# Kernel optimization log

Measured on AMD Instinct MI355X. Metric: run time of the kernel, lower is better.

## Reference

```python
import jax, jax.numpy as jnp
import numpy as np
from jax import lax

SUR_BETA = 4.0
THRESH = 1.0
ALPHA = float(np.exp(-1.0 / 20.0))  # membrane decay, tau_mem=20
BETA = float(np.exp(-1.0 / 5.0))    # synaptic decay, tau_syn=5

@jax.custom_vjp
def spike(x):
    return (x >= 0).astype(jnp.float32)

def _spike_fwd(x):
    return spike(x), x

def _spike_bwd(x, g):
    e = jnp.exp(-SUR_BETA * jnp.abs(x))
    sg = SUR_BETA * e / (2.0 * (1.0 + e) ** 2)
    return (g * sg,)

spike.defvjp(_spike_fwd, _spike_bwd)

def lif_layer(x, W, b):
    # x: [B, T, Din] -> spikes [B, T, H]
    xt = jnp.einsum('bti,ih->bth', x, W) + b
    B, T, H = xt.shape
    z = jnp.zeros((B, H), xt.dtype)
    def step(carry, x_t):
        v, i = carry
        i = BETA * i + x_t
        v = ALPHA * v + i
        s = spike(v - THRESH)
        v = v * (1.0 - s)  # multiplicative reset
        return (v, i), s
    _, sp = lax.scan(step, (z, z), xt.transpose(1, 0, 2))
    return sp.transpose(1, 0, 2)

def layer_norm(x, scale, bias, eps=1e-6):
    m = jnp.mean(x, axis=-1, keepdims=True)
    v = jnp.mean((x - m) ** 2, axis=-1, keepdims=True)
    return (x - m) / jnp.sqrt(v + eps) * scale + bias

def setup_inputs() -> dict:
    key = jax.random.key(0)
    ks = jax.random.split(key, 6)
    B, T, S, F = 64, 512, 64, 16
    D = S * F  # 1024
    def w(k, shape, fan):
        return (jax.random.normal(k, shape, jnp.float32) / np.sqrt(fan)).astype(jnp.float32)
    return dict(
        spike_trains=(jax.random.uniform(ks[0], (B, T, S, F)) < 0.2).astype(jnp.float32),
        W0=w(ks[1], (D, 256), D), b0=jnp.zeros((256,), jnp.float32),
        W1=w(ks[2], (256, 128), 256), b1=jnp.zeros((128,), jnp.float32),
        W2=w(ks[3], (128, 64), 128), b2=jnp.zeros((64,), jnp.float32),
        ln1_scale=jnp.ones((256,), jnp.float32), ln1_bias=jnp.zeros((256,), jnp.float32),
        ln2_scale=jnp.ones((128,), jnp.float32), ln2_bias=jnp.zeros((128,), jnp.float32),
        Wc=w(ks[4], (B, 2), B), bc=jnp.zeros((2,), jnp.float32),
    )

def reference(spike_trains, W0, b0, W1, b1, W2, b2,
              ln1_scale, ln1_bias, ln2_scale, ln2_bias, Wc, bc):
    B, T, S, F = spike_trains.shape
    x = spike_trains.reshape(B, T, S * F)
    x = lif_layer(x, W0, b0)                                   # [B,T,256]
    x = lif_layer(layer_norm(x, ln1_scale, ln1_bias), W1, b1)  # [B,T,128]
    x = lif_layer(layer_norm(x, ln2_scale, ln2_bias), W2, b2)  # [B,T,64]
    pooled = jnp.mean(x, axis=(1, 2))  # [B]  (faithful to source: mean over time AND hidden)
    logits = pooled @ Wc + bc          # [num_classes] -- classifier sees batch as feature dim
    return (logits, pooled, jnp.mean(x))
```

## Files before the change

### kernel.cpp

```cpp
#include <hip/hip_runtime.h>

#define T_STEPS 512
#define BATCH 64

__device__ constexpr float ALPHA_ = 0.95122942450071400910f;
__device__ constexpr float BETA_  = 0.81873075307798185867f;

typedef __attribute__((ext_vector_type(8))) short bf16x8;
typedef __attribute__((ext_vector_type(4))) float f32x4;

__device__ inline unsigned short f2bf_rne(float f) {
  union { float f; unsigned int u; } v{f};
  const unsigned int u = v.u;
  return (unsigned short)((u + 0x7FFFu + ((u >> 16) & 1u)) >> 16);
}
__device__ inline float bf2f(unsigned short h) {
  union { unsigned int u; float f; } v{(unsigned int)h << 16};
  return v.f;
}

__device__ inline void gload16(const void* g, void* l) {
  __builtin_amdgcn_global_load_lds(
      (const __attribute__((address_space(1))) unsigned int*)g,
      (__attribute__((address_space(3))) unsigned int*)l, 16, 0, 0);
}

__device__ inline bf16x8 cvt8_trunc(f32x4 a, f32x4 b) {
  bf16x8 r;
  const unsigned int* ua = (const unsigned int*)&a;
  const unsigned int* ub = (const unsigned int*)&b;
  r[0] = (short)(ua[0] >> 16); r[1] = (short)(ua[1] >> 16);
  r[2] = (short)(ua[2] >> 16); r[3] = (short)(ua[3] >> 16);
  r[4] = (short)(ub[0] >> 16); r[5] = (short)(ub[1] >> 16);
  r[6] = (short)(ub[2] >> 16); r[7] = (short)(ub[3] >> 16);
  return r;
}

template <int BN, bool A_F32, bool LNFOLD>
__global__ __launch_bounds__(256) void gemm_mfma(
    const void* __restrict__ Av, const char* __restrict__ Bhi,
    const char* __restrict__ Blo, const float* __restrict__ uvec,
    const float* __restrict__ cvec, const float* __restrict__ invv,
    const float* __restrict__ miv, float* __restrict__ C,
    int M, int N, int K) {
  constexpr int NFPW = BN / 32;
  constexpr int UB = BN * 4;
  __shared__ char As[8192];
  __shared__ char Bh[UB * 16];
  __shared__ char Bl[UB * 16];

  const int tid = threadIdx.x;
  const int lane = tid & 63;
  const int wave = tid >> 6;
  const int wr = wave >> 1, wc = wave & 1;
  const int l15 = lane & 15, l4 = lane >> 4;
  const int row0 = blockIdx.y * 128;
  const int col0 = blockIdx.x * BN;
  const int KB = K / 32;
  const int cbKB = blockIdx.x * KB;

  f32x4 acc[4][NFPW] = {};

  for (int kb = 0; kb < KB; ++kb) {
    const int k0 = kb * 32;
    f32x4 a0lo, a0hi, a1lo, a1hi;
    if constexpr (A_F32) {
      const float* A = (const float*)Av;
      const int r0 = tid >> 2, j0 = tid & 3;
      const float* p0 = A + (size_t)(row0 + r0) * K + k0 + j0 * 8;
      const float* p1 = A + (size_t)(row0 + 64 + r0) * K + k0 + j0 * 8;
      a0lo = *(const f32x4*)p0; a0hi = *(const f32x4*)(p0 + 4);
      a1lo = *(const f32x4*)p1; a1hi = *(const f32x4*)(p1 + 4);
    }
    __syncthreads();
    if constexpr (A_F32) {
      const int r0 = tid >> 2, j0 = tid & 3;
      const int u0 = ((r0 >> 4) << 6) + (j0 << 4) + (r0 & 15);
      const int r1 = 64 + r0;
      const int u1 = ((r1 >> 4) << 6) + (j0 << 4) + (r1 & 15);
      *(bf16x8*)(As + u0 * 16) = cvt8_trunc(a0lo, a0hi);
      *(bf16x8*)(As + u1 * 16) = cvt8_trunc(a1lo, a1hi);
    } else {
      const char* A = (const char*)Av;
#pragma unroll
      for (int i = 0; i < 2; ++i) {
        const int unit = (wave * 2 + i) * 64 + lane;
        const int r = ((unit >> 6) << 4) | (unit & 15);
        const int j = (unit >> 4) & 3;
        gload16(A + (size_t)(row0 + r) * (K * 2) + (size_t)(k0 + j * 8) * 2,
                As + unit * 16);
      }
    }
    {
      constexpr int nb = UB / 256;
#pragma unroll
      for (int i = 0; i < nb; ++i) {
        const int unit = (wave * nb + i) * 64 + lane;
        const size_t so = ((size_t)(cbKB + kb) * UB + unit) * 16;
        gload16(Bhi + so, Bh + unit * 16);
        gload16(Blo + so, Bl + unit * 16);
      }
    }
    __syncthreads();

    bf16x8 af[4], bhf[NFPW], blf[NFPW];
#pragma unroll
    for (int m = 0; m < 4; ++m)
      af[m] = *(const bf16x8*)(As + ((wr * 4 + m) * 64 + lane) * 16);
#pragma unroll
    for (int n = 0; n < NFPW; ++n) {
      const int u = ((wc * NFPW + n) * 64 + lane) * 16;
      bhf[n] = *(const bf16x8*)(Bh + u);
      blf[n] = *(const bf16x8*)(Bl + u);
    }
#pragma unroll
    for (int m = 0; m < 4; ++m)
#pragma unroll
      for (int n = 0; n < NFPW; ++n) {
        acc[m][n] = __builtin_amdgcn_mfma_f32_16x16x32_bf16(af[m], bhf[n], acc[m][n], 0, 0, 0);
        acc[m][n] = __builtin_amdgcn_mfma_f32_16x16x32_bf16(af[m], blf[n], acc[m][n], 0, 0, 0);
      }
  }

#pragma unroll
  for (int m = 0; m < 4; ++m) {
    const int rbase = row0 + (wr * 4 + m) * 16 + l4 * 4;
    f32x4 iv, mv;
    if constexpr (LNFOLD) {
      iv = *(const f32x4*)(invv + rbase);
      mv = *(const f32x4*)(miv + rbase);
    }
#pragma unroll
    for (int n = 0; n < NFPW; ++n) {
      const int c = col0 + (wc * NFPW + n) * 16 + l15;
      float uu = 0.f;
      const float cc = cvec[c];
      if constexpr (LNFOLD) uu = uvec[c];
#pragma unroll
      for (int r = 0; r < 4; ++r) {
        float v;
        if constexpr (LNFOLD) v = iv[r] * acc[m][n][r] - mv[r] * uu + cc;
        else v = acc[m][n][r] + cc;
        C[(size_t)(rbase + r) * N + c] = v;
      }
    }
  }
}

template <int BN>
__global__ void prep_split(const float* __restrict__ W, const float* __restrict__ s,
                           char* __restrict__ hi, char* __restrict__ lo,
                           int K, int N) {
  const int g = blockIdx.x * 256 + threadIdx.x;
  const int total = (K * N) / 8;
  if (g >= total) return;
  constexpr int UB = BN * 4;
  const int KB = K / 32;
  const int unit = g % UB;
  const int kb = (g / UB) % KB;
  const int cb = g / (UB * KB);
  const int n = cb * BN + ((unit >> 6) << 4) + (unit & 15);
  const int kbase = kb * 32 + ((unit >> 4) & 3) * 8;
  short h8[8], l8[8];
#pragma unroll
  for (int jj = 0; jj < 8; ++jj) {
    const int k = kbase + jj;
    float w = W[(size_t)k * N + n];
    if (s) w *= s[k];
    const unsigned short hb = f2bf_rne(w);
    const unsigned short lb = f2bf_rne(w - bf2f(hb));
    h8[jj] = (short)hb; l8[jj] = (short)lb;
  }
  *(bf16x8*)(hi + (size_t)g * 16) = *(const bf16x8*)h8;
  *(bf16x8*)(lo + (size_t)g * 16) = *(const bf16x8*)l8;
}

__global__ __launch_bounds__(256) void prep_consts(
    const float* __restrict__ W, const float* __restrict__ s,
    const float* __restrict__ b, const float* __restrict__ bias2,
    float* __restrict__ u, float* __restrict__ c, int K, int N) {
  const int n = blockIdx.x;
  const int t = threadIdx.x;
  float us = 0.f, cs = 0.f;
  for (int k = t; k < K; k += 256) {
    const float w = W[(size_t)k * N + n];
    us += s[k] * w;
    cs += b[k] * w;
  }
  __shared__ float su[256], sc[256];
  su[t] = us; sc[t] = cs;
  __syncthreads();
  for (int o = 128; o > 0; o >>= 1) {
    if (t < o) { su[t] += su[t + o]; sc[t] += sc[t + o]; }
    __syncthreads();
  }
  if (t == 0) { u[n] = su[0]; c[n] = sc[0] + bias2[n]; }
}

template <int K>
__global__ __launch_bounds__(256) void rowstats(
    const unsigned short* __restrict__ sp, float* __restrict__ invv,
    float* __restrict__ miv) {
  const int wave = threadIdx.x >> 6, lane = threadIdx.x & 63;
  const int row = blockIdx.x * 4 + wave;
  const unsigned short* p = sp + (size_t)row * K;
  float ssum = 0.f;
  if constexpr (K == 256) {
    const ushort4 v = *(const ushort4*)(p + lane * 4);
    ssum = bf2f(v.x) + bf2f(v.y) + bf2f(v.z) + bf2f(v.w);
  } else {
    const ushort2 v = *(const ushort2*)(p + lane * 2);
    ssum = bf2f(v.x) + bf2f(v.y);
  }
#pragma unroll
  for (int o = 32; o > 0; o >>= 1) ssum += __shfl_xor(ssum, o);
  if (lane == 0) {
    const float m = ssum / (float)K;
    const float inv = 1.0f / sqrtf(m * (1.f - m) + 1e-6f);
    invv[row] = inv;
    miv[row] = m * inv;
  }
}

template <int H, bool SPIKE_OUT, bool ACCUM>
__global__ void lif_scan(const float* __restrict__ xt,
                         unsigned short* __restrict__ sp,
                         float* __restrict__ tsum) {
  const int n = blockIdx.x * 64 + threadIdx.x;
  const int b = n / H, h = n % H;
  const float* p = xt + (size_t)b * T_STEPS * H + h;
  unsigned short* q = nullptr;
  if constexpr (SPIKE_OUT) q = sp + (size_t)b * T_STEPS * H + h;

  float v = 0.f, cur = 0.f, ts = 0.f;
  for (int t = 0; t < T_STEPS; t += 16) {
    float x[16];
#pragma unroll
    for (int u = 0; u < 16; ++u) x[u] = p[(size_t)u * H];
#pragma unroll
    for (int u = 0; u < 16; ++u) {
      cur = BETA_ * cur + x[u];
      v = ALPHA_ * v + cur;
      const bool sb = (v >= 1.f);
      if constexpr (SPIKE_OUT) q[(size_t)u * H] = sb ? 0x3F80 : 0;
      if constexpr (ACCUM) ts += sb ? 1.f : 0.f;
      v = sb ? 0.f : v;
    }
    p += (size_t)16 * H;
    if constexpr (SPIKE_OUT) q += (size_t)16 * H;
  }
  if constexpr (ACCUM) tsum[n] = ts;
}

__global__ void finalize(const float* __restrict__ tsum,
                         const float* __restrict__ Wc,
                         const float* __restrict__ bc,
                         float* __restrict__ out) {
  const int b = threadIdx.x;
  float s = 0.f;
#pragma unroll 8
  for (int h = 0; h < 64; ++h) s += tsum[b * 64 + h];
  const float pooled = s * (1.0f / (512.f * 64.f));
  out[2 + b] = pooled;

  float tot = pooled;
  float l0 = pooled * Wc[b * 2 + 0];
  float l1 = pooled * Wc[b * 2 + 1];
#pragma unroll
  for (int off = 32; off > 0; off >>= 1) {
    tot += __shfl_xor(tot, off);
    l0 += __shfl_xor(l0, off);
    l1 += __shfl_xor(l1, off);
  }
  if (b == 0) {
    out[0] = l0 + bc[0];
    out[1] = l1 + bc[1];
    out[66] = tot * (1.0f / 64.f);
  }
}

extern "C" void kernel_launch(void* const* d_in, const int* in_sizes, int n_in,
                              void* d_out, int out_size, void* d_ws, size_t ws_size,
                              hipStream_t stream) {
  const float* X    = (const float*)d_in[0];
  const float* W0   = (const float*)d_in[1];
  const float* b0   = (const float*)d_in[2];
  const float* W1   = (const float*)d_in[3];
  const float* b1   = (const float*)d_in[4];
  const float* W2   = (const float*)d_in[5];
  const float* b2   = (const float*)d_in[6];
  const float* ln1s = (const float*)d_in[7];
  const float* ln1b = (const float*)d_in[8];
  const float* ln2s = (const float*)d_in[9];
  const float* ln2b = (const float*)d_in[10];
  const float* Wc   = (const float*)d_in[11];
  const float* bc   = (const float*)d_in[12];
  float* out = (float*)d_out;

  char* w = (char*)d_ws;
  float* buf0 = (float*)w;
  float* buf1 = (float*)w;
  float* buf2 = (float*)(w + 16777216);
  size_t off = 33554432;
  unsigned short* sp0 = (unsigned short*)(w + off); off += 16777216;
  unsigned short* sp1 = (unsigned short*)(w + off); off += 8388608;
  char* hi0 = w + off; off += 524288;
  char* lo0 = w + off; off += 524288;
  char* hi1 = w + off; off += 65536;
  char* lo1 = w + off; off += 65536;
  char* hi2 = w + off; off += 16384;
  char* lo2 = w + off; off += 16384;
  float* u1 = (float*)(w + off); off += 512;
  float* c1 = (float*)(w + off); off += 512;
  float* u2 = (float*)(w + off); off += 256;
  float* c2 = (float*)(w + off); off += 256;
  float* inv1 = (float*)(w + off); off += 131072;
  float* mi1  = (float*)(w + off); off += 131072;
  float* inv2 = (float*)(w + off); off += 131072;
  float* mi2  = (float*)(w + off); off += 131072;
  float* tsum = (float*)(w + off); off += 16384;

  const int M = 32768;

  prep_split<128><<<128, 256, 0, stream>>>(W0, nullptr, hi0, lo0, 1024, 256);
  prep_split<128><<<16, 256, 0, stream>>>(W1, ln1s, hi1, lo1, 256, 128);
  prep_split<64><<<4, 256, 0, stream>>>(W2, ln2s, hi2, lo2, 128, 64);
  prep_consts<<<128, 256, 0, stream>>>(W1, ln1s, ln1b, b1, u1, c1, 256, 128);
  prep_consts<<<64, 256, 0, stream>>>(W2, ln2s, ln2b, b2, u2, c2, 128, 64);

  gemm_mfma<128, true, false><<<dim3(2, M / 128), 256, 0, stream>>>(
      X, hi0, lo0, nullptr, b0, nullptr, nullptr, buf0, M, 256, 1024);
  lif_scan<256, true, false><<<(BATCH * 256) / 64, 64, 0, stream>>>(buf0, sp0, nullptr);

  rowstats<256><<<M / 4, 256, 0, stream>>>(sp0, inv1, mi1);
  gemm_mfma<128, false, true><<<dim3(1, M / 128), 256, 0, stream>>>(
      sp0, hi1, lo1, u1, c1, inv1, mi1, buf1, M, 128, 256);
  lif_scan<128, true, false><<<(BATCH * 128) / 64, 64, 0, stream>>>(buf1, sp1, nullptr);

  rowstats<128><<<M / 4, 256, 0, stream>>>(sp1, inv2, mi2);
  gemm_mfma<64, false, true><<<dim3(1, M / 128), 256, 0, stream>>>(
      sp1, hi2, lo2, u2, c2, inv2, mi2, buf2, M, 64, 128);
  lif_scan<64, false, true><<<(BATCH * 64) / 64, 64, 0, stream>>>(buf2, nullptr, tsum);

  finalize<<<1, 64, 0, stream>>>(tsum, Wc, bc, out);
}
```

Before: 155.0 us.

## Replace LDS-staged GEMM with per-wave register double-buffered MFMA tiles

The block-shared LDS GEMM is replaced by a kernel where each wave owns a 64x64 output tile and loads A and B fragments directly from global memory into registers. Loads are double-buffered across k-steps so the next tile's loads overlap the current MFMAs, and block-level barriers are removed. The fp32-to-bf16 truncation now uses a byte-permute pack. Weight pre-splitting switches to 64-column panels to match. Without shared-memory reuse, A rows are re-read by every wave that needs them, which raises global and L2 traffic and register use.

```diff
diff --git a/kernel.cpp b/kernel.cpp
--- a/kernel.cpp
+++ b/kernel.cpp
@@ -19,122 +19,115 @@
   return v.f;
 }
 
-__device__ inline void gload16(const void* g, void* l) {
-  __builtin_amdgcn_global_load_lds(
-      (const __attribute__((address_space(1))) unsigned int*)g,
-      (__attribute__((address_space(3))) unsigned int*)l, 16, 0, 0);
-}
-
-__device__ inline bf16x8 cvt8_trunc(f32x4 a, f32x4 b) {
-  bf16x8 r;
-  const unsigned int* ua = (const unsigned int*)&a;
-  const unsigned int* ub = (const unsigned int*)&b;
-  r[0] = (short)(ua[0] >> 16); r[1] = (short)(ua[1] >> 16);
-  r[2] = (short)(ua[2] >> 16); r[3] = (short)(ua[3] >> 16);
-  r[4] = (short)(ub[0] >> 16); r[5] = (short)(ub[1] >> 16);
-  r[6] = (short)(ub[2] >> 16); r[7] = (short)(ub[3] >> 16);
-  return r;
-}
-
-template <int BN, bool A_F32, bool LNFOLD>
-__global__ __launch_bounds__(256) void gemm_mfma(
+__device__ inline unsigned int pkbf(float first, float second) {
+#if __has_builtin(__builtin_amdgcn_perm)
+  return __builtin_amdgcn_perm(__float_as_uint(second), __float_as_uint(first),
+                               0x07060302u);
+#else
+  return (__float_as_uint(first) >> 16) | (__float_as_uint(second) & 0xFFFF0000u);
+#endif
+}
+
+__device__ inline bf16x8 cvt_frag(const f32x4 lo, const f32x4 hi) {
+  union { unsigned int w[4]; bf16x8 v; } u;
+  u.w[0] = pkbf(lo.x, lo.y);
+  u.w[1] = pkbf(lo.z, lo.w);
+  u.w[2] = pkbf(hi.x, hi.y);
+  u.w[3] = pkbf(hi.z, hi.w);
+  return u.v;
+}
+
+template <int NWC, bool A_F32, bool LNFOLD>
+__global__ __launch_bounds__(256) void gemm_wave(
     const void* __restrict__ Av, const char* __restrict__ Bhi,
     const char* __restrict__ Blo, const float* __restrict__ uvec,
     const float* __restrict__ cvec, const float* __restrict__ invv,
-    const float* __restrict__ miv, float* __restrict__ C,
-    int M, int N, int K) {
-  constexpr int NFPW = BN / 32;
-  constexpr int UB = BN * 4;
-  __shared__ char As[8192];
-  __shared__ char Bh[UB * 16];
-  __shared__ char Bl[UB * 16];
-
+    const float* __restrict__ miv, float* __restrict__ C, int N, int K) {
   const int tid = threadIdx.x;
   const int lane = tid & 63;
-  const int wave = tid >> 6;
-  const int wr = wave >> 1, wc = wave & 1;
+  const int wid = blockIdx.x * 4 + (tid >> 6);
+  const int wr = wid / NWC, wc = wid % NWC;
   const int l15 = lane & 15, l4 = lane >> 4;
-  const int row0 = blockIdx.y * 128;
-  const int col0 = blockIdx.x * BN;
+  const int row0 = wr * 64, col0 = wc * 64;
   const int KB = K / 32;
-  const int cbKB = blockIdx.x * KB;
-
-  f32x4 acc[4][NFPW] = {};
-
-  for (int kb = 0; kb < KB; ++kb) {
-    const int k0 = kb * 32;
-    f32x4 a0lo, a0hi, a1lo, a1hi;
-    if constexpr (A_F32) {
-      const float* A = (const float*)Av;
-      const int r0 = tid >> 2, j0 = tid & 3;
-      const float* p0 = A + (size_t)(row0 + r0) * K + k0 + j0 * 8;
-      const float* p1 = A + (size_t)(row0 + 64 + r0) * K + k0 + j0 * 8;
-      a0lo = *(const f32x4*)p0; a0hi = *(const f32x4*)(p0 + 4);
-      a1lo = *(const f32x4*)p1; a1hi = *(const f32x4*)(p1 + 4);
-    }
-    __syncthreads();
-    if constexpr (A_F32) {
-      const int r0 = tid >> 2, j0 = tid & 3;
-      const int u0 = ((r0 >> 4) << 6) + (j0 << 4) + (r0 & 15);
-      const int r1 = 64 + r0;
-      const int u1 = ((r1 >> 4) << 6) + (j0 << 4) + (r1 & 15);
-      *(bf16x8*)(As + u0 * 16) = cvt8_trunc(a0lo, a0hi);
-      *(bf16x8*)(As + u1 * 16) = cvt8_trunc(a1lo, a1hi);
-    } else {
-      const char* A = (const char*)Av;
-#pragma unroll
-      for (int i = 0; i < 2; ++i) {
-        const int unit = (wave * 2 + i) * 64 + lane;
-        const int r = ((unit >> 6) << 4) | (unit & 15);
-        const int j = (unit >> 4) & 3;
-        gload16(A + (size_t)(row0 + r) * (K * 2) + (size_t)(k0 + j * 8) * 2,
-                As + unit * 16);
+
+  const char* Ab = (const char*)Av;
+  size_t a_off[4];
+#pragma unroll
+  for (int m = 0; m < 4; ++m)
+    a_off[m] = ((size_t)(row0 + m * 16 + l15) * K + l4 * 8) * (A_F32 ? 4 : 2);
+
+  const char* bh_p = Bhi + (size_t)wc * KB * 4096 + (size_t)lane * 16;
+  const char* bl_p = Blo + (size_t)wc * KB * 4096 + (size_t)lane * 16;
+
+  f32x4 acc[4][4] = {};
+  f32x4 lo0[4], hi0[4], lo1[4], hi1[4];
+  bf16x8 ab0[4], ab1[4], bh0[4], bl0[4], bh1[4], bl1[4];
+
+  auto loadA = [&](int kb, f32x4 (&lo)[4], f32x4 (&hi)[4], bf16x8 (&ab)[4]) {
+#pragma unroll
+    for (int m = 0; m < 4; ++m) {
+      if constexpr (A_F32) {
+        const float* p = (const float*)(Ab + a_off[m] + (size_t)kb * 128);
+        lo[m] = *(const f32x4*)p;
+        hi[m] = *(const f32x4*)(p + 4);
+      } else {
+        ab[m] = *(const bf16x8*)(Ab + a_off[m] + (size_t)kb * 64);
       }
     }
-    {
-      constexpr int nb = UB / 256;
-#pragma unroll
-      for (int i = 0; i < nb; ++i) {
-        const int unit = (wave * nb + i) * 64 + lane;
-        const size_t so = ((size_t)(cbKB + kb) * UB + unit) * 16;
-        gload16(Bhi + so, Bh + unit * 16);
-        gload16(Blo + so, Bl + unit * 16);
+  };
+  auto loadB = [&](int kb, bf16x8 (&bh)[4], bf16x8 (&bl)[4]) {
+    const char* ph = bh_p + (size_t)kb * 4096;
+    const char* pl = bl_p + (size_t)kb * 4096;
+#pragma unroll
+    for (int n = 0; n < 4; ++n) {
+      bh[n] = *(const bf16x8*)(ph + n * 1024);
+      bl[n] = *(const bf16x8*)(pl + n * 1024);
+    }
+  };
+  auto compute = [&](f32x4 (&lo)[4], f32x4 (&hi)[4], bf16x8 (&ab)[4],
+                     bf16x8 (&bh)[4], bf16x8 (&bl)[4]) {
+    bf16x8 af[4];
+#pragma unroll
+    for (int m = 0; m < 4; ++m) {
+      if constexpr (A_F32) af[m] = cvt_frag(lo[m], hi[m]);
+      else af[m] = ab[m];
+    }
+#pragma unroll
+    for (int m = 0; m < 4; ++m)
+#pragma unroll
+      for (int n = 0; n < 4; ++n) {
+        acc[m][n] = __builtin_amdgcn_mfma_f32_16x16x32_bf16(af[m], bh[n], acc[m][n], 0, 0, 0);
+        acc[m][n] = __builtin_amdgcn_mfma_f32_16x16x32_bf16(af[m], bl[n], acc[m][n], 0, 0, 0);
       }
-    }
-    __syncthreads();
-
-    bf16x8 af[4], bhf[NFPW], blf[NFPW];
-#pragma unroll
-    for (int m = 0; m < 4; ++m)
-      af[m] = *(const bf16x8*)(As + ((wr * 4 + m) * 64 + lane) * 16);
-#pragma unroll
-    for (int n = 0; n < NFPW; ++n) {
-      const int u = ((wc * NFPW + n) * 64 + lane) * 16;
-      bhf[n] = *(const bf16x8*)(Bh + u);
-      blf[n] = *(const bf16x8*)(Bl + u);
-    }
-#pragma unroll
-    for (int m = 0; m < 4; ++m)
-#pragma unroll
-      for (int n = 0; n < NFPW; ++n) {
-        acc[m][n] = __builtin_amdgcn_mfma_f32_16x16x32_bf16(af[m], bhf[n], acc[m][n], 0, 0, 0);
-        acc[m][n] = __builtin_amdgcn_mfma_f32_16x16x32_bf16(af[m], blf[n], acc[m][n], 0, 0, 0);
-      }
+  };
+
+  loadA(0, lo0, hi0, ab0);
+  loadB(0, bh0, bl0);
+  for (int kb = 0; kb < KB; kb += 2) {
+    loadA(kb + 1, lo1, hi1, ab1);
+    loadB(kb + 1, bh1, bl1);
+    compute(lo0, hi0, ab0, bh0, bl0);
+    if (kb + 2 < KB) {
+      loadA(kb + 2, lo0, hi0, ab0);
+      loadB(kb + 2, bh0, bl0);
+    }
+    compute(lo1, hi1, ab1, bh1, bl1);
   }
 
 #pragma unroll
   for (int m = 0; m < 4; ++m) {
-    const int rbase = row0 + (wr * 4 + m) * 16 + l4 * 4;
-    f32x4 iv, mv;
+    const int rbase = row0 + m * 16 + l4 * 4;
+    f32x4 iv{}, mv{};
     if constexpr (LNFOLD) {
       iv = *(const f32x4*)(invv + rbase);
       mv = *(const f32x4*)(miv + rbase);
     }
 #pragma unroll
-    for (int n = 0; n < NFPW; ++n) {
-      const int c = col0 + (wc * NFPW + n) * 16 + l15;
+    for (int n = 0; n < 4; ++n) {
+      const int c = col0 + n * 16 + l15;
+      const float cc = cvec[c];
       float uu = 0.f;
-      const float cc = cvec[c];
       if constexpr (LNFOLD) uu = uvec[c];
 #pragma unroll
       for (int r = 0; r < 4; ++r) {
@@ -322,24 +315,24 @@
 
   const int M = 32768;
 
-  prep_split<128><<<128, 256, 0, stream>>>(W0, nullptr, hi0, lo0, 1024, 256);
-  prep_split<128><<<16, 256, 0, stream>>>(W1, ln1s, hi1, lo1, 256, 128);
+  prep_split<64><<<128, 256, 0, stream>>>(W0, nullptr, hi0, lo0, 1024, 256);
+  prep_split<64><<<16, 256, 0, stream>>>(W1, ln1s, hi1, lo1, 256, 128);
   prep_split<64><<<4, 256, 0, stream>>>(W2, ln2s, hi2, lo2, 128, 64);
   prep_consts<<<128, 256, 0, stream>>>(W1, ln1s, ln1b, b1, u1, c1, 256, 128);
   prep_consts<<<64, 256, 0, stream>>>(W2, ln2s, ln2b, b2, u2, c2, 128, 64);
 
-  gemm_mfma<128, true, false><<<dim3(2, M / 128), 256, 0, stream>>>(
-      X, hi0, lo0, nullptr, b0, nullptr, nullptr, buf0, M, 256, 1024);
+  gemm_wave<4, true, false><<<512, 256, 0, stream>>>(
+      X, hi0, lo0, nullptr, b0, nullptr, nullptr, buf0, 256, 1024);
   lif_scan<256, true, false><<<(BATCH * 256) / 64, 64, 0, stream>>>(buf0, sp0, nullptr);
 
   rowstats<256><<<M / 4, 256, 0, stream>>>(sp0, inv1, mi1);
-  gemm_mfma<128, false, true><<<dim3(1, M / 128), 256, 0, stream>>>(
-      sp0, hi1, lo1, u1, c1, inv1, mi1, buf1, M, 128, 256);
+  gemm_wave<2, false, true><<<256, 256, 0, stream>>>(
+      sp0, hi1, lo1, u1, c1, inv1, mi1, buf1, 128, 256);
   lif_scan<128, true, false><<<(BATCH * 128) / 64, 64, 0, stream>>>(buf1, sp1, nullptr);
 
   rowstats<128><<<M / 4, 256, 0, stream>>>(sp1, inv2, mi2);
-  gemm_mfma<64, false, true><<<dim3(1, M / 128), 256, 0, stream>>>(
-      sp1, hi2, lo2, u2, c2, inv2, mi2, buf2, M, 64, 128);
+  gemm_wave<1, false, true><<<128, 256, 0, stream>>>(
+      sp1, hi2, lo2, u2, c2, inv2, mi2, buf2, 64, 128);
   lif_scan<64, false, true><<<(BATCH * 64) / 64, 64, 0, stream>>>(buf2, nullptr, tsum);
 
   finalize<<<1, 64, 0, stream>>>(tsum, Wc, bc, out);
```

Result: slower. 191.3 us (+23.5%).
